# Performance work log

Measured on AMD Instinct MI355X. Metric: run time of the kernel, lower is better.

## Reference

```python
import jax, jax.numpy as jnp
import numpy as np
import math

SR = 16000
FFT = 1024
WIN = 640
HOP = 320
NMEL = 40
NCEP = 13
B = 1024
NS = 16000
F_MIN = 0.0
F_MAX = 8000.0
LIFT_L = 22.0
DELTA_N = 2


def _linear_to_mel_weight_matrix(num_mel, num_spec_bins, sr, fmin, fmax):
    # Exact replica of tf.signal.linear_to_mel_weight_matrix (HTK mel scale).
    def hz_to_mel(f):
        return 1127.0 * np.log1p(np.asarray(f, np.float64) / 700.0)
    nyquist = sr / 2.0
    lin_freqs = np.linspace(0.0, nyquist, num_spec_bins)
    spec_mel = hz_to_mel(lin_freqs[1:])[:, None]          # drop DC bin
    edges = np.linspace(hz_to_mel(fmin), hz_to_mel(fmax), num_mel + 2)
    lower, center, upper = edges[:-2], edges[1:-1], edges[2:]
    lower_slope = (spec_mel - lower) / (center - lower)
    upper_slope = (upper - spec_mel) / (upper - center)
    w = np.maximum(0.0, np.minimum(lower_slope, upper_slope))
    w = np.pad(w, ((1, 0), (0, 0)))                       # re-add zero DC row
    return w.astype(np.float32)


def setup_inputs() -> dict:
    key = jax.random.key(0)
    waveforms = jax.random.normal(key, (B, NS), dtype=jnp.float32)
    mel_fb = jnp.asarray(_linear_to_mel_weight_matrix(NMEL, FFT // 2 + 1, SR, F_MIN, F_MAX))
    return {"waveforms": waveforms, "mel_fb": mel_fb}


def _delta(feat, N):
    # feat: (B, T, C). Replicate-pad N frames at both ends, then weighted
    # sliding-window sum with weights k in [-N..N] (vectorized, no map_fn).
    T = feat.shape[1]
    denom = 2.0 * sum(float(k * k) for k in range(1, N + 1))
    padded = jnp.concatenate(
        [jnp.repeat(feat[:, :1, :], N, axis=1), feat,
         jnp.repeat(feat[:, -1:, :], N, axis=1)], axis=1)
    acc = jnp.zeros_like(feat)
    for k in range(-N, N + 1):
        if k != 0:
            acc = acc + float(k) * padded[:, N + k:N + k + T, :]
    return acc / denom


def reference(waveforms, mel_fb):
    # --- STFT (tf.signal.stft: periodic Hann, no pad_end, zero-pad to FFT) ---
    n = jnp.arange(WIN, dtype=jnp.float32)
    window = 0.5 - 0.5 * jnp.cos(2.0 * math.pi * n / WIN)
    num_frames = 1 + (NS - WIN) // HOP                    # 49
    idx = jnp.arange(num_frames)[:, None] * HOP + jnp.arange(WIN)[None, :]
    frames = waveforms[:, idx] * window
    frames = jnp.pad(frames, ((0, 0), (0, 0), (0, FFT - WIN)))
    spec = jnp.abs(jnp.fft.rfft(frames, n=FFT, axis=-1))  # (B, T, 513)

    # --- mel + log ---
    log_mel = jnp.log(spec @ mel_fb + 1e-6)               # (B, T, NMEL)

    # --- MFCC: DCT-II scaled by rsqrt(2*NMEL), keep first NCEP coeffs ---
    m = jnp.arange(NMEL, dtype=jnp.float32)[:, None]
    k = jnp.arange(NCEP, dtype=jnp.float32)[None, :]
    dct_mat = 2.0 * jnp.cos(math.pi * (2.0 * m + 1.0) * k / (2.0 * NMEL))
    mfccs = (log_mel @ dct_mat) * (1.0 / math.sqrt(2.0 * NMEL))

    # --- liftering ---
    c = jnp.arange(NCEP, dtype=jnp.float32)
    lift = 1.0 + (LIFT_L / 2.0) * jnp.sin(math.pi * c / LIFT_L)
    mfccs = mfccs * lift

    # --- deltas and delta-deltas ---
    d1 = _delta(mfccs, DELTA_N)
    d2 = _delta(d1, DELTA_N)
    out = jnp.concatenate([mfccs, d1, d2], axis=2)        # (B, T, 3*NCEP)
    return out[..., None]                                 # (B, T, 39, 1)
```

## Files before the change

kernel.cpp:

```cpp
#include <hip/hip_runtime.h>
#include <math.h>

#define NMEL   40
#define NCEP   13
#define BATCH  1024
#define NSAMP  16000
#define NFRAME 49
#define PI_F   3.14159265358979323846f

#define WS_WIN  0
#define WS_R    640
#define WS_DT   1664
#define WS_BT   2184
#define WS_TOT  15240

typedef _Float16 half8 __attribute__((ext_vector_type(8)));
typedef __fp16   fp16x2 __attribute__((ext_vector_type(2)));
typedef float f32x4 __attribute__((ext_vector_type(4)));

#define WAVE_FENCE() { __builtin_amdgcn_wave_barrier(); asm volatile("" ::: "memory"); }

#define BFLY(i0, i1, wr, wi) {                        \
    float tr = zr[i0] - zr[i1], ti = zi[i0] - zi[i1]; \
    zr[i0] += zr[i1]; zi[i0] += zi[i1];               \
    zr[i1] = tr*(wr) - ti*(wi);                       \
    zi[i1] = tr*(wi) + ti*(wr); }

__device__ __forceinline__ unsigned pk_f16(float a, float b) {
    fp16x2 h = __builtin_amdgcn_cvt_pkrtz(a, b);
    union { fp16x2 h; unsigned u; } cvt; cvt.h = h;
    return cvt.u;
}

__global__ __launch_bounds__(256) void mfcc_prep(
    const float* __restrict__ mel_fb, float* __restrict__ ws)
{
    const int idx = blockIdx.x * 256 + threadIdx.x;

    _Float16* bt = (_Float16*)(ws + WS_BT);
    for (int i = idx; i < 48 * 544; i += 64 * 256) {
        int n = i / 544, k = i - n * 544;
        float v = (n < NMEL && k < 513) ? mel_fb[k * NMEL + n] : 0.0f;
        bt[i] = (_Float16)v;
    }

    if (idx < 640 + 512 + 520) {
        int i = idx;
        if (i < 640) {
            ws[WS_WIN + i] = 0.5f - 0.5f * cosf(2.0f * PI_F * (float)i / 640.0f);
        } else if (i < 1152) {
            int k = i - 640;
            float s, c;
            sincosf(-2.0f * PI_F * (float)k / 1024.0f, &s, &c);
            ((float2*)(ws + WS_R))[k] = make_float2(c, s);
        } else {
            int j = i - 1152;
            int m = j / 13, c0 = j - m * 13;
            float d    = 2.0f * cosf(PI_F * (2.0f * m + 1.0f) * (float)c0 / 80.0f);
            float lift = 1.0f + 11.0f * sinf(PI_F * (float)c0 / 22.0f);
            ws[WS_DT + j] = d * 0.11180339887498949f * lift;
        }
    }
}

__global__ __launch_bounds__(256) void mfcc_stage1(
    const float* __restrict__ wave, const float* __restrict__ ws,
    float* __restrict__ out)
{
    __shared__ __align__(16) char smem[4 * 640 * 8 + 16 * 40 * 2];
    char* smemc = smem;
    _Float16* lm = (_Float16*)(smem + 4 * 640 * 8);

    const int tid = threadIdx.x;
    const int wv  = tid >> 6;
    const int L   = tid & 63;
    const int s   = L & 7;
    const int a   = L >> 3;

    float2* Z = (float2*)smem + wv * 640;
    const float2* R   = (const float2*)(ws + WS_R);
    const float2* win = (const float2*)(ws + WS_WIN);

    float2 twA[4], twB[2], twC, twD[4], twE[2], twF, twS[8], winv[5];
    #pragma unroll
    for (int j = 0; j < 4; ++j) twA[j] = R[2 * (L + 64 * j)];
    #pragma unroll
    for (int j = 0; j < 2; ++j) twB[j] = R[4 * (L + 64 * j)];
    twC = R[8 * L];
    #pragma unroll
    for (int j = 0; j < 4; ++j) twD[j] = R[128 * j + 16 * s];
    #pragma unroll
    for (int j = 0; j < 2; ++j) twE[j] = R[256 * j + 32 * s];
    twF = R[64 * s];
    #pragma unroll
    for (int j = 0; j < 8; ++j) twS[j] = R[8 * L + j];
    #pragma unroll
    for (int j = 0; j < 5; ++j) winv[j] = win[L + 64 * j];

    uint4 mgp[4];
    float m512v[4] = {0.0f, 0.0f, 0.0f, 0.0f};

    #pragma unroll
    for (int fi = 0; fi < 4; ++fi) {
        const int frame = blockIdx.x * 16 + wv * 4 + fi;
        const int b = frame / NFRAME;
        const int f = frame - b * NFRAME;
        const float2* xin = (const float2*)(wave + (size_t)b * NSAMP + (size_t)f * 320);

        float zr[8], zi[8];
        #pragma unroll
        for (int j = 0; j < 8; ++j) { zr[j] = 0.0f; zi[j] = 0.0f; }
        #pragma unroll
        for (int j = 0; j < 5; ++j) {
            float2 x = xin[L + 64 * j];
            zr[j] = x.x * winv[j].x;
            zi[j] = x.y * winv[j].y;
        }

        #pragma unroll
        for (int j = 0; j < 4; ++j) BFLY(j, j + 4, twA[j].x, twA[j].y);
        #pragma unroll
        for (int g = 0; g < 8; g += 4) {
            #pragma unroll
            for (int j = 0; j < 2; ++j) BFLY(g + j, g + j + 2, twB[j].x, twB[j].y);
        }
        #pragma unroll
        for (int i0 = 0; i0 < 8; i0 += 2) BFLY(i0, i0 + 1, twC.x, twC.y);

        WAVE_FENCE();
        #pragma unroll
        for (int j = 0; j < 8; ++j)
            Z[80 * j + 10 * s + a] = make_float2(zr[j], zi[j]);
        WAVE_FENCE();
        {
            float4 q0 = *(float4*)&Z[10 * L + 0];
            float4 q1 = *(float4*)&Z[10 * L + 2];
            float4 q2 = *(float4*)&Z[10 * L + 4];
            float4 q3 = *(float4*)&Z[10 * L + 6];
            zr[0] = q0.x; zi[0] = q0.y; zr[1] = q0.z; zi[1] = q0.w;
            zr[2] = q1.x; zi[2] = q1.y; zr[3] = q1.z; zi[3] = q1.w;
            zr[4] = q2.x; zi[4] = q2.y; zr[5] = q2.z; zi[5] = q2.w;
            zr[6] = q3.x; zi[6] = q3.y; zr[7] = q3.z; zi[7] = q3.w;
        }

        #pragma unroll
        for (int j = 0; j < 4; ++j) BFLY(j, j + 4, twD[j].x, twD[j].y);
        #pragma unroll
        for (int g = 0; g < 8; g += 4) {
            #pragma unroll
            for (int j = 0; j < 2; ++j) BFLY(g + j, g + j + 2, twE[j].x, twE[j].y);
        }
        #pragma unroll
        for (int i0 = 0; i0 < 8; i0 += 2) BFLY(i0, i0 + 1, twF.x, twF.y);

        WAVE_FENCE();
        #pragma unroll
        for (int j = 0; j < 8; ++j)
            Z[80 * a + 10 * j + s] = make_float2(zr[j], zi[j]);
        WAVE_FENCE();
        {
            float4 q0 = *(float4*)&Z[10 * L + 0];
            float4 q1 = *(float4*)&Z[10 * L + 2];
            float4 q2 = *(float4*)&Z[10 * L + 4];
            float4 q3 = *(float4*)&Z[10 * L + 6];
            zr[0] = q0.x; zi[0] = q0.y; zr[1] = q0.z; zi[1] = q0.w;
            zr[2] = q1.x; zi[2] = q1.y; zr[3] = q1.z; zi[3] = q1.w;
            zr[4] = q2.x; zi[4] = q2.y; zr[5] = q2.z; zi[5] = q2.w;
            zr[6] = q3.x; zi[6] = q3.y; zr[7] = q3.z; zi[7] = q3.w;
        }

        {
            const float C = 0.70710678118654752f;
            const float w8r[4] = { 1.0f,  C, 0.0f, -C };
            const float w8i[4] = { 0.0f, -C, -1.0f, -C };
            #pragma unroll
            for (int j = 0; j < 4; ++j) BFLY(j, j + 4, w8r[j], w8i[j]);
            #pragma unroll
            for (int g = 0; g < 8; g += 4) {
                BFLY(g + 0, g + 2, 1.0f, 0.0f);
                BFLY(g + 1, g + 3, 0.0f, -1.0f);
            }
            #pragma unroll
            for (int i0 = 0; i0 < 8; i0 += 2) BFLY(i0, i0 + 1, 1.0f, 0.0f);
        }

        WAVE_FENCE();
        {
            const int rev3t[8] = { 0, 4, 2, 6, 1, 5, 3, 7 };
            int r6 = (int)(__brev((unsigned)L) >> 26);
            int u  = r6 + 2 * (r6 >> 3);
            #pragma unroll
            for (int j = 0; j < 8; ++j)
                Z[80 * rev3t[j] + u] = make_float2(zr[j], zi[j]);
        }
        WAVE_FENCE();

        float Ax[8], Ay[8], Bx[8], By[8];
        {
            float4 a0 = *(float4*)&Z[10 * L + 0];
            float4 a1 = *(float4*)&Z[10 * L + 2];
            float4 a2 = *(float4*)&Z[10 * L + 4];
            float4 a3 = *(float4*)&Z[10 * L + 6];
            Ax[0] = a0.x; Ay[0] = a0.y; Ax[1] = a0.z; Ay[1] = a0.w;
            Ax[2] = a1.x; Ay[2] = a1.y; Ax[3] = a1.z; Ay[3] = a1.w;
            Ax[4] = a2.x; Ay[4] = a2.y; Ax[5] = a2.z; Ay[5] = a2.w;
            Ax[6] = a3.x; Ay[6] = a3.y; Ax[7] = a3.z; Ay[7] = a3.w;
            float4 t0 = *(float4*)&Z[630 - 10 * L + 0];
            float4 t1 = *(float4*)&Z[630 - 10 * L + 2];
            float4 t2 = *(float4*)&Z[630 - 10 * L + 4];
            float4 t3 = *(float4*)&Z[630 - 10 * L + 6];
            float2 b0 = Z[640 - 10 * L];
            Bx[0] = b0.x;  By[0] = b0.y;
            Bx[7] = t0.z;  By[7] = t0.w;
            Bx[6] = t1.x;  By[6] = t1.y;
            Bx[5] = t1.z;  By[5] = t1.w;
            Bx[4] = t2.x;  By[4] = t2.y;
            Bx[3] = t2.z;  By[3] = t2.w;
            Bx[2] = t3.x;  By[2] = t3.y;
            Bx[1] = t3.z;  By[1] = t3.w;
        }
        float mg[8];
        #pragma unroll
        for (int j = 0; j < 8; ++j) {
            int k = 8 * L + j;
            if (k == 0) {
                mg[j]     = fabsf(Ax[0] + Ay[0]);
                m512v[fi] = fabsf(Ax[0] - Ay[0]);
            } else {
                float xer = 0.5f * (Ax[j] + Bx[j]), xei = 0.5f * (Ay[j] - By[j]);
                float xo  = 0.5f * (Ay[j] + By[j]), xoi = -0.5f * (Ax[j] - Bx[j]);
                float xr = xer + twS[j].x * xo - twS[j].y * xoi;
                float xi = xei + twS[j].x * xoi + twS[j].y * xo;
                mg[j] = sqrtf(xr * xr + xi * xi);
            }
        }
        mgp[fi].x = pk_f16(mg[0], mg[1]);
        mgp[fi].y = pk_f16(mg[2], mg[3]);
        mgp[fi].z = pk_f16(mg[4], mg[5]);
        mgp[fi].w = pk_f16(mg[6], mg[7]);
        WAVE_FENCE();
    }

    __syncthreads();
    #pragma unroll
    for (int fi = 0; fi < 4; ++fi) {
        const int row = wv * 4 + fi;
        *(uint4*)(smemc + row * 1104 + 16 * L) = mgp[fi];
        if (L < 20) {
            unsigned v = (L == 0) ? pk_f16(m512v[fi], 0.0f) : 0u;
            *(unsigned*)(smemc + row * 1104 + 1024 + 4 * L) = v;
        }
    }
    __syncthreads();

    if (wv < 3) {
        const int nl = L & 15, q = L >> 4;
        const char* ap = smemc + nl * 1104 + q * 16;
        const _Float16* btp = (const _Float16*)(ws + WS_BT)
                              + (size_t)(wv * 16 + nl) * 544 + q * 8;
        f32x4 acc = {0.0f, 0.0f, 0.0f, 0.0f};
        #pragma unroll
        for (int kk = 0; kk < 17; ++kk) {
            half8 av = *(const half8*)(ap + kk * 64);
            half8 bv = *(const half8*)(btp + kk * 32);
            acc = __builtin_amdgcn_mfma_f32_16x16x32_f16(av, bv, acc, 0, 0, 0);
        }
        const int mel = wv * 16 + nl;
        if (mel < NMEL) {
            #pragma unroll
            for (int r = 0; r < 4; ++r) {
                int fl = q * 4 + r;
                lm[fl * NMEL + mel] = (_Float16)__logf(acc[r] + 1e-6f);
            }
        }
    }
    __syncthreads();

    if (tid < 16 * NCEP) {
        const int fl = tid / NCEP, c = tid - fl * NCEP;
        float acc = 0.0f;
        #pragma unroll
        for (int m = 0; m < NMEL; ++m)
            acc += (float)lm[fl * NMEL + m] * ws[WS_DT + m * 13 + c];
        out[(size_t)(blockIdx.x * 16 + fl) * (3 * NCEP) + c] = acc;
    }
}

__global__ __launch_bounds__(128) void mfcc_stage2(float* __restrict__ out)
{
    __shared__ float x [NFRAME * NCEP];
    __shared__ float d1[NFRAME * NCEP];

    const int b = blockIdx.x;
    const int tid = threadIdx.x;
    const int TC = NFRAME * NCEP;

    for (int i = tid; i < TC; i += 128) {
        const int t = i / NCEP, c = i - t * NCEP;
        x[i] = out[((size_t)b * NFRAME + t) * (3 * NCEP) + c];
    }
    __syncthreads();

    for (int i = tid; i < TC; i += 128) {
        const int t = i / NCEP, c = i - t * NCEP;
        float acc = 0.0f;
        #pragma unroll
        for (int k = -2; k <= 2; ++k) {
            if (k == 0) continue;
            int tt = t + k;
            tt = tt < 0 ? 0 : (tt > NFRAME - 1 ? NFRAME - 1 : tt);
            acc += (float)k * x[tt * NCEP + c];
        }
        d1[i] = acc * 0.1f;
    }
    __syncthreads();

    for (int i = tid; i < TC; i += 128) {
        const int t = i / NCEP, c = i - t * NCEP;
        float acc = 0.0f;
        #pragma unroll
        for (int k = -2; k <= 2; ++k) {
            if (k == 0) continue;
            int tt = t + k;
            tt = tt < 0 ? 0 : (tt > NFRAME - 1 ? NFRAME - 1 : tt);
            acc += (float)k * d1[tt * NCEP + c];
        }
        const size_t base = ((size_t)b * NFRAME + t) * (3 * NCEP);
        out[base +     NCEP + c] = d1[i];
        out[base + 2 * NCEP + c] = acc * 0.1f;
    }
}

extern "C" void kernel_launch(void* const* d_in, const int* in_sizes, int n_in,
                              void* d_out, int out_size, void* d_ws, size_t ws_size,
                              hipStream_t stream)
{
    const float* wave   = (const float*)d_in[0];
    const float* mel_fb = (const float*)d_in[1];
    float* out = (float*)d_out;
    float* ws  = (float*)d_ws;

    mfcc_prep<<<64, 256, 0, stream>>>(mel_fb, ws);
    mfcc_stage1<<<(BATCH * NFRAME) / 16, 256, 0, stream>>>(wave, ws, out);
    mfcc_stage2<<<BATCH, 128, 0, stream>>>(out);
}
```

Measured before the change: 175.2 us.

## Prefetch next frame's samples into registers and relax intra-wave FFT fences

The frame loop now double-buffers the waveform input in registers. The next frame's samples are loaded while the current frame's FFT runs, so global-load latency overlaps with butterfly work. The wave-barrier-plus-memory-clobber fences are replaced with sched_barrier masks that keep LDS operations in place but let VALU and VMEM move across them. A minimum-blocks-per-CU hint is added to launch bounds. These add register pressure, and dropping the compiler memory clobber risks IR-level reordering of the cross-lane LDS exchanges.

Measured after the change: 269.7 us. +53.9%, slower.

```diff
diff --git a/kernel.cpp b/kernel.cpp
--- a/kernel.cpp
+++ b/kernel.cpp
@@ -18,7 +18,7 @@
 typedef __fp16   fp16x2 __attribute__((ext_vector_type(2)));
 typedef float f32x4 __attribute__((ext_vector_type(4)));
 
-#define WAVE_FENCE() { __builtin_amdgcn_wave_barrier(); asm volatile("" ::: "memory"); }
+#define FFT_SB() __builtin_amdgcn_sched_barrier(0x77)
 
 #define BFLY(i0, i1, wr, wi) {                        \
     float tr = zr[i0] - zr[i1], ti = zi[i0] - zi[i1]; \
@@ -63,7 +63,7 @@
     }
 }
 
-__global__ __launch_bounds__(256) void mfcc_stage1(
+__global__ __launch_bounds__(256, 5) void mfcc_stage1(
     const float* __restrict__ wave, const float* __restrict__ ws,
     float* __restrict__ out)
 {
@@ -100,21 +100,35 @@
     uint4 mgp[4];
     float m512v[4] = {0.0f, 0.0f, 0.0f, 0.0f};
 
-    #pragma unroll
-    for (int fi = 0; fi < 4; ++fi) {
-        const int frame = blockIdx.x * 16 + wv * 4 + fi;
+    float2 xv[5];
+    {
+        const int frame = blockIdx.x * 16 + wv * 4;
         const int b = frame / NFRAME;
         const int f = frame - b * NFRAME;
-        const float2* xin = (const float2*)(wave + (size_t)b * NSAMP + (size_t)f * 320);
+        const float2* xp = (const float2*)(wave + (size_t)b * NSAMP + (size_t)f * 320);
+        #pragma unroll
+        for (int j = 0; j < 5; ++j) xv[j] = xp[L + 64 * j];
+    }
+
+    #pragma unroll
+    for (int fi = 0; fi < 4; ++fi) {
+        float2 xn[5];
+        if (fi < 3) {
+            const int frame = blockIdx.x * 16 + wv * 4 + fi + 1;
+            const int b = frame / NFRAME;
+            const int f = frame - b * NFRAME;
+            const float2* xp = (const float2*)(wave + (size_t)b * NSAMP + (size_t)f * 320);
+            #pragma unroll
+            for (int j = 0; j < 5; ++j) xn[j] = xp[L + 64 * j];
+        }
 
         float zr[8], zi[8];
         #pragma unroll
         for (int j = 0; j < 8; ++j) { zr[j] = 0.0f; zi[j] = 0.0f; }
         #pragma unroll
         for (int j = 0; j < 5; ++j) {
-            float2 x = xin[L + 64 * j];
-            zr[j] = x.x * winv[j].x;
-            zi[j] = x.y * winv[j].y;
+            zr[j] = xv[j].x * winv[j].x;
+            zi[j] = xv[j].y * winv[j].y;
         }
 
         #pragma unroll
@@ -127,11 +141,11 @@
         #pragma unroll
         for (int i0 = 0; i0 < 8; i0 += 2) BFLY(i0, i0 + 1, twC.x, twC.y);
 
-        WAVE_FENCE();
+        FFT_SB();
         #pragma unroll
         for (int j = 0; j < 8; ++j)
             Z[80 * j + 10 * s + a] = make_float2(zr[j], zi[j]);
-        WAVE_FENCE();
+        FFT_SB();
         {
             float4 q0 = *(float4*)&Z[10 * L + 0];
             float4 q1 = *(float4*)&Z[10 * L + 2];
@@ -153,11 +167,11 @@
         #pragma unroll
         for (int i0 = 0; i0 < 8; i0 += 2) BFLY(i0, i0 + 1, twF.x, twF.y);
 
-        WAVE_FENCE();
+        FFT_SB();
         #pragma unroll
         for (int j = 0; j < 8; ++j)
             Z[80 * a + 10 * j + s] = make_float2(zr[j], zi[j]);
-        WAVE_FENCE();
+        FFT_SB();
         {
             float4 q0 = *(float4*)&Z[10 * L + 0];
             float4 q1 = *(float4*)&Z[10 * L + 2];
@@ -184,7 +198,7 @@
             for (int i0 = 0; i0 < 8; i0 += 2) BFLY(i0, i0 + 1, 1.0f, 0.0f);
         }
 
-        WAVE_FENCE();
+        FFT_SB();
         {
             const int rev3t[8] = { 0, 4, 2, 6, 1, 5, 3, 7 };
             int r6 = (int)(__brev((unsigned)L) >> 26);
@@ -193,7 +207,7 @@
             for (int j = 0; j < 8; ++j)
                 Z[80 * rev3t[j] + u] = make_float2(zr[j], zi[j]);
         }
-        WAVE_FENCE();
+        FFT_SB();
 
         float Ax[8], Ay[8], Bx[8], By[8];
         {
@@ -238,7 +252,12 @@
         mgp[fi].y = pk_f16(mg[2], mg[3]);
         mgp[fi].z = pk_f16(mg[4], mg[5]);
         mgp[fi].w = pk_f16(mg[6], mg[7]);
-        WAVE_FENCE();
+        FFT_SB();
+
+        if (fi < 3) {
+            #pragma unroll
+            for (int j = 0; j < 5; ++j) xv[j] = xn[j];
+        }
     }
 
     __syncthreads();
```
